# Performance work log

Hardware: AMD Instinct MI355X
Metric: run time of the kernel (lower is better)

## Reference

```python
import jax, jax.numpy as jnp
import numpy as np

VOCAB = 14
EMBED = 10
HIDDEN = 50
MLP = 50
PAD_IDX = 0
BATCH = 4096
SEQ = 2048


def setup_inputs() -> dict:
    key = jax.random.key(0)
    ks = jax.random.split(key, 10)
    tokens = jax.random.randint(ks[0], (BATCH, SEQ), 0, VOCAB, dtype=jnp.int64 if jax.config.jax_enable_x64 else jnp.int32)
    s_lstm = 1.0 / np.sqrt(HIDDEN)
    s_mlp1 = 1.0 / np.sqrt(HIDDEN)
    s_mlp2 = 1.0 / np.sqrt(MLP)
    emb = jax.random.normal(ks[1], (VOCAB, EMBED), jnp.float32)
    emb = emb.at[PAD_IDX].set(0.0)  # padding_idx row is zero in torch Embedding
    W_ih = jax.random.uniform(ks[2], (4 * HIDDEN, EMBED), jnp.float32, -s_lstm, s_lstm)
    W_hh = jax.random.uniform(ks[3], (4 * HIDDEN, HIDDEN), jnp.float32, -s_lstm, s_lstm)
    b_ih = jax.random.uniform(ks[4], (4 * HIDDEN,), jnp.float32, -s_lstm, s_lstm)
    b_hh = jax.random.uniform(ks[5], (4 * HIDDEN,), jnp.float32, -s_lstm, s_lstm)
    W1 = jax.random.uniform(ks[6], (MLP, HIDDEN), jnp.float32, -s_mlp1, s_mlp1)
    b1 = jax.random.uniform(ks[7], (MLP,), jnp.float32, -s_mlp1, s_mlp1)
    W2 = jax.random.uniform(ks[8], (1, MLP), jnp.float32, -s_mlp2, s_mlp2)
    b2 = jax.random.uniform(ks[9], (1,), jnp.float32, -s_mlp2, s_mlp2)
    return {"input": tokens, "emb": emb, "W_ih": W_ih, "W_hh": W_hh,
            "b_ih": b_ih, "b_hh": b_hh, "W1": W1, "b1": b1, "W2": W2, "b2": b2}


def reference(input, emb, W_ih, W_hh, b_ih, b_hh, W1, b1, W2, b2):
    x = emb[input]                                   # [B, T, E]
    mask = (input != PAD_IDX).astype(emb.dtype)      # [B, T]
    xs = jnp.swapaxes(x, 0, 1)                       # [T, B, E]
    ms = jnp.swapaxes(mask, 0, 1)[:, :, None]        # [T, B, 1]
    B = input.shape[0]

    def step(carry, inp):
        h, c = carry
        xt, mt = inp
        gates = xt @ W_ih.T + b_ih + h @ W_hh.T + b_hh  # [B, 4H], order i,f,g,o
        i, f, g, o = jnp.split(gates, 4, axis=-1)
        i = jax.nn.sigmoid(i)
        f = jax.nn.sigmoid(f)
        g = jnp.tanh(g)
        o = jax.nn.sigmoid(o)
        c_new = f * c + i * g
        h_new = o * jnp.tanh(c_new)
        # blend: keep old state on padded positions
        h = h_new * mt + h * (1.0 - mt)
        c = c_new * mt + c * (1.0 - mt)
        return (h, c), None

    h0 = jnp.zeros((B, HIDDEN), emb.dtype)
    c0 = jnp.zeros((B, HIDDEN), emb.dtype)
    (h, c), _ = jax.lax.scan(step, (h0, c0), (xs, ms))
    hidden = h @ W1.T + b1                            # [B, MLP]
    out = jax.nn.sigmoid(hidden @ W2.T + b2)          # [B, 1]
    return out
```

## Files before the change

kernel.cpp:

```cpp
#include <hip/hip_runtime.h>

#define BATCH 4096
#define SEQ   2048
#define EMB   10
#define HID   50
#define VOCAB 14
#define NTILE 13
#define TROW  2052

using bf16x8 = __attribute__((ext_vector_type(8))) short;
using f32x4  = __attribute__((ext_vector_type(4))) float;

__device__ __forceinline__ short f2bf(float f) {
  unsigned u = __builtin_bit_cast(unsigned, f);
  u = (u + 0x7FFFu + ((u >> 16) & 1u)) >> 16;
  return (short)u;
}
__device__ __forceinline__ float fsigm(float x) {
  return __builtin_amdgcn_rcpf(1.0f + __builtin_amdgcn_exp2f(x * -1.44269504f));
}

__global__ void prep_kernel(const float* __restrict__ emb,  const float* __restrict__ W_ih,
                            const float* __restrict__ W_hh, const float* __restrict__ b_ih,
                            const float* __restrict__ b_hh, short* __restrict__ Apack) {
  int idx = blockIdx.x * 256 + threadIdx.x;
  if (idx >= NTILE * 2 * 64 * 8) return;
  int j    = idx & 7;
  int lane = (idx >> 3) & 63;
  int kf   = (idx >> 9) & 1;
  int t    = idx >> 10;
  int m    = lane & 15;
  int q    = m >> 2, g = m & 3;
  int jh   = 13 * q + t;
  int k    = kf * 32 + (lane >> 4) * 8 + j;
  float v = 0.0f;
  if (jh < HID) {
    int R = g * HID + jh;
    float scale = (g == 2) ? -2.885390082f : -1.442695041f;
    if (k < HID) {
      v = W_hh[R * HID + k] * scale;
    } else {
      int vo = k - HID;
      float s = b_ih[R] + b_hh[R];
      for (int e = 0; e < EMB; ++e) s += emb[vo * EMB + e] * W_ih[R * EMB + e];
      v = s * scale;
    }
  }
  Apack[idx] = f2bf(v);
}

__global__ __launch_bounds__(512, 1) void lstm_kernel(
    const int* __restrict__ tokens, const short* __restrict__ Apack,
    const float* __restrict__ W1, const float* __restrict__ b1,
    const float* __restrict__ W2, const float* __restrict__ b2,
    float* __restrict__ out) {
  __shared__ __align__(16) unsigned char toku8[16 * TROW];
  __shared__ __align__(16) short hbuf[2][16 * 64];
  __shared__ float hfin[16 * 52];
  __shared__ float mlp_hid[16 * 52];

  const int tid  = threadIdx.x;
  const int lane = tid & 63;
  const int wv   = tid >> 6;
  const int b0   = blockIdx.x * 16;
  const int bB   = lane & 15;
  const int jj   = lane >> 4;
  const bool two = (wv < 5);
  const int jh0  = 13 * jj + wv;
  const int jh1  = 13 * jj + wv + 8;
  const bool hval1 = two && (jh1 < HID);

  const int ohi   = (wv - 5) * 64 + lane;
  const bool ohact = (wv == 5 || wv == 6) && (ohi < 112);
  const int ohr   = ohi / 7;
  const int ohsub = ohi % 7;
  const int ohoct = (ohsub < 3) ? 6 : 7;
  const int ohinn = (ohsub < 3) ? (4 + 4 * ohsub) : (4 * (ohsub - 3));
  const int ohb   = ohr * 128 + 16 * ((ohoct + ohr) & 7) + ohinn;
  const int ohv0  = 2 * ohsub, ohv1 = 2 * ohsub + 1;

  bf16x8 Af00 = {}, Af01 = {}, Af10 = {}, Af11 = {};
  Af00 = *(const bf16x8*)(Apack + ((wv * 2 + 0) * 64 + lane) * 8);
  Af01 = *(const bf16x8*)(Apack + ((wv * 2 + 1) * 64 + lane) * 8);
  if (two) {
    Af10 = *(const bf16x8*)(Apack + (((wv + 8) * 2 + 0) * 64 + lane) * 8);
    Af11 = *(const bf16x8*)(Apack + (((wv + 8) * 2 + 1) * 64 + lane) * 8);
  }

  for (int i = tid; i < 16 * 512; i += 512) {
    int row = i >> 9, c4 = i & 511;
    int4 tv = *(const int4*)&tokens[(b0 + row) * SEQ + 4 * c4];
    unsigned pk = (tv.x & 0xFF) | ((tv.y & 0xFF) << 8) |
                  ((tv.z & 0xFF) << 16) | ((tv.w & 0xFF) << 24);
    *(unsigned*)&toku8[row * TROW + 4 * c4] = pk;
  }
  for (int i = tid; i < 1024; i += 512) hbuf[0][i] = 0;
  __syncthreads();

  char* hb = (char*)hbuf;
  const int rb0  = bB * 128 + 16 * ((jj + bB) & 7);
  const int rb1  = bB * 128 + 16 * (((jj + 4) + bB) & 7);
  const int hwb0 = bB * 128 + 16 * (((jh0 >> 3) + bB) & 7) + 2 * (jh0 & 7);
  const int hwb1 = bB * 128 + 16 * (((jh1 >> 3) + bB) & 7) + 2 * (jh1 & 7);
  const unsigned char* myrow = &toku8[bB * TROW];
  const unsigned char* ohtok = &toku8[ohr * TROW];

  if (ohact) {
    int tk = ohtok[0];
    unsigned wb = ((tk == ohv0) ? 0x3F80u : 0u) | ((tk == ohv1) ? 0x3F800000u : 0u);
    *(unsigned*)(hb + ohb) = wb;
  }

  float c0 = 0.f, h0 = 0.f, c1 = 0.f, h1 = 0.f;
  unsigned mp = 0;

#define CELL(ACC, C, H)                                                        \
  {                                                                            \
    float eA = __builtin_amdgcn_exp2f(ACC[0]);                                 \
    float eB = __builtin_amdgcn_exp2f(ACC[1]);                                 \
    float eC = __builtin_amdgcn_exp2f(ACC[2]);                                 \
    float eG = __builtin_amdgcn_exp2f(ACC[3]);                                 \
    float a1 = 1.0f + eA, bb1 = 1.0f + eB, cc1 = 1.0f + eC, g1 = 1.0f + eG;    \
    float P   = a1 * cc1;                                                      \
    float t1  = __builtin_fmaf(-eC, bb1, bb1);                                 \
    float num = __builtin_fmaf(C, P, t1);                                      \
    float den = P * bb1;                                                       \
    float cn  = num * __builtin_amdgcn_rcpf(den);                              \
    cn = fminf(fmaxf(cn, -30.0f), 30.0f);                                      \
    float eH  = __builtin_amdgcn_exp2f(cn * -2.885390082f);                    \
    float hd  = g1 * (1.0f + eH);                                              \
    float hn  = (1.0f - eH) * __builtin_amdgcn_rcpf(hd);                       \
    C = keep ? cn : C;                                                         \
    H = keep ? hn : H;                                                         \
  }

  for (int t = 0; t < SEQ; t += 16) {
#pragma unroll
    for (int u = 0; u < 16; ++u) {
      const int T  = t + u;
      const int PB = (u & 1) * 2048, PN = PB ^ 2048;
      __syncthreads();

      bf16x8 Bf0 = *(const bf16x8*)(hb + PB + rb0);
      bf16x8 Bf1 = *(const bf16x8*)(hb + PB + rb1);
      if ((u & 3) == 0) mp = *(const unsigned*)(myrow + T);

      f32x4 acc0 = {0.f, 0.f, 0.f, 0.f};
      acc0 = __builtin_amdgcn_mfma_f32_16x16x32_bf16(Af00, Bf0, acc0, 0, 0, 0);
      acc0 = __builtin_amdgcn_mfma_f32_16x16x32_bf16(Af01, Bf1, acc0, 0, 0, 0);
      f32x4 acc1 = {0.f, 0.f, 0.f, 0.f};
      if (two) {
        acc1 = __builtin_amdgcn_mfma_f32_16x16x32_bf16(Af10, Bf0, acc1, 0, 0, 0);
        acc1 = __builtin_amdgcn_mfma_f32_16x16x32_bf16(Af11, Bf1, acc1, 0, 0, 0);
      }

      if (ohact && T + 1 < SEQ) {
        int tk = ohtok[T + 1];
        unsigned wb = ((tk == ohv0) ? 0x3F80u : 0u) |
                      ((tk == ohv1) ? 0x3F800000u : 0u);
        *(unsigned*)(hb + PN + ohb) = wb;
      }

      const bool keep = (((mp >> (8 * (u & 3))) & 0xFF) != 0);
      CELL(acc0, c0, h0)
      *(short*)(hb + PN + hwb0) = f2bf(h0);
      if (two) {
        CELL(acc1, c1, h1)
        if (hval1) *(short*)(hb + PN + hwb1) = f2bf(h1);
      }
    }
  }
#undef CELL

  hfin[bB * 52 + jh0] = h0;
  if (hval1) hfin[bB * 52 + jh1] = h1;
  __syncthreads();
  for (int idx = tid; idx < 16 * 64; idx += 512) {
    int b = idx >> 6, m = idx & 63;
    if (m < HID) {
      float s = b1[m];
      for (int j2 = 0; j2 < HID; ++j2) s += hfin[b * 52 + j2] * W1[m * HID + j2];
      mlp_hid[b * 52 + m] = s;
    }
  }
  __syncthreads();
  if (tid < 16) {
    float s = b2[0];
    for (int m2 = 0; m2 < HID; ++m2) s += mlp_hid[tid * 52 + m2] * W2[m2];
    out[b0 + tid] = fsigm(s);
  }
}

extern "C" void kernel_launch(void* const* d_in, const int* in_sizes, int n_in,
                              void* d_out, int out_size, void* d_ws, size_t ws_size,
                              hipStream_t stream) {
  const int*   tokens = (const int*)  d_in[0];
  const float* emb    = (const float*)d_in[1];
  const float* W_ih   = (const float*)d_in[2];
  const float* W_hh   = (const float*)d_in[3];
  const float* b_ih   = (const float*)d_in[4];
  const float* b_hh   = (const float*)d_in[5];
  const float* W1     = (const float*)d_in[6];
  const float* b1     = (const float*)d_in[7];
  const float* W2     = (const float*)d_in[8];
  const float* b2     = (const float*)d_in[9];
  float* outp  = (float*)d_out;
  short* Apack = (short*)d_ws;

  hipLaunchKernelGGL(prep_kernel, dim3(52), dim3(256), 0, stream,
                     emb, W_ih, W_hh, b_ih, b_hh, Apack);
  hipLaunchKernelGGL(lstm_kernel, dim3(BATCH / 16), dim3(512), 0, stream,
                     tokens, Apack, W1, b1, W2, b2, outp);
}
```

Baseline: 852.1 us.

## Remap hidden units so paired waves write packed bf16 pairs and share reciprocals

```diff
diff --git a/kernel.cpp b/kernel.cpp
--- a/kernel.cpp
+++ b/kernel.cpp
@@ -5,7 +5,6 @@
 #define EMB   10
 #define HID   50
 #define VOCAB 14
-#define NTILE 13
 #define TROW  2052
 
 using bf16x8 = __attribute__((ext_vector_type(8))) short;
@@ -16,6 +15,9 @@
   u = (u + 0x7FFFu + ((u >> 16) & 1u)) >> 16;
   return (short)u;
 }
+__device__ __forceinline__ unsigned f2bf2(float lo, float hi) {
+  return (unsigned)(unsigned short)f2bf(lo) | ((unsigned)(unsigned short)f2bf(hi) << 16);
+}
 __device__ __forceinline__ float fsigm(float x) {
   return __builtin_amdgcn_rcpf(1.0f + __builtin_amdgcn_exp2f(x * -1.44269504f));
 }
@@ -24,14 +26,15 @@
                             const float* __restrict__ W_hh, const float* __restrict__ b_ih,
                             const float* __restrict__ b_hh, short* __restrict__ Apack) {
   int idx = blockIdx.x * 256 + threadIdx.x;
-  if (idx >= NTILE * 2 * 64 * 8) return;
+  if (idx >= 13 * 2 * 64 * 8) return;
   int j    = idx & 7;
   int lane = (idx >> 3) & 63;
   int kf   = (idx >> 9) & 1;
-  int t    = idx >> 10;
+  int tid  = idx >> 10;
   int m    = lane & 15;
   int q    = m >> 2, g = m & 3;
-  int jh   = 13 * q + t;
+  int jh   = (tid < 10) ? (2 * ((tid >> 1) * 4 + q) + (tid & 1))
+                        : (40 + (tid - 10) * 4 + q);
   int k    = kf * 32 + (lane >> 4) * 8 + j;
   float v = 0.0f;
   if (jh < HID) {
@@ -65,27 +68,30 @@
   const int b0   = blockIdx.x * 16;
   const int bB   = lane & 15;
   const int jj   = lane >> 4;
-  const bool two = (wv < 5);
-  const int jh0  = 13 * jj + wv;
-  const int jh1  = 13 * jj + wv + 8;
-  const bool hval1 = two && (jh1 < HID);
-
-  const int ohi   = (wv - 5) * 64 + lane;
-  const bool ohact = (wv == 5 || wv == 6) && (ohi < 112);
-  const int ohr   = ohi / 7;
-  const int ohsub = ohi % 7;
+
+  const bool two = (0xA7 >> wv) & 1;
+  const int  fr  = __builtin_popcount(0xA7 & ((1 << wv) - 1));
+  const int  sr  = __builtin_popcount(0x58 & ((1 << wv) - 1));
+  const int  p   = fr * 4 + jj;
+  const int  jhS = 40 + sr * 4 + jj;
+  const bool sval = !two && (jhS < HID);
+
+  const int t0 = two ? (fr * 2) : (10 + sr);
+  bf16x8 Af00 = *(const bf16x8*)(Apack + ((t0 * 2 + 0) * 64 + lane) * 8);
+  bf16x8 Af01 = *(const bf16x8*)(Apack + ((t0 * 2 + 1) * 64 + lane) * 8);
+  bf16x8 Af10 = {}, Af11 = {};
+  if (two) {
+    Af10 = *(const bf16x8*)(Apack + (((t0 + 1) * 2 + 0) * 64 + lane) * 8);
+    Af11 = *(const bf16x8*)(Apack + (((t0 + 1) * 2 + 1) * 64 + lane) * 8);
+  }
+
+  const bool ohact = (wv == 3 || wv == 4) && (lane < 56);
+  const int ohr   = (wv - 3) * 8 + lane / 7;
+  const int ohsub = lane % 7;
   const int ohoct = (ohsub < 3) ? 6 : 7;
   const int ohinn = (ohsub < 3) ? (4 + 4 * ohsub) : (4 * (ohsub - 3));
   const int ohb   = ohr * 128 + 16 * ((ohoct + ohr) & 7) + ohinn;
   const int ohv0  = 2 * ohsub, ohv1 = 2 * ohsub + 1;
-
-  bf16x8 Af00 = {}, Af01 = {}, Af10 = {}, Af11 = {};
-  Af00 = *(const bf16x8*)(Apack + ((wv * 2 + 0) * 64 + lane) * 8);
-  Af01 = *(const bf16x8*)(Apack + ((wv * 2 + 1) * 64 + lane) * 8);
-  if (two) {
-    Af10 = *(const bf16x8*)(Apack + (((wv + 8) * 2 + 0) * 64 + lane) * 8);
-    Af11 = *(const bf16x8*)(Apack + (((wv + 8) * 2 + 1) * 64 + lane) * 8);
-  }
 
   for (int i = tid; i < 16 * 512; i += 512) {
     int row = i >> 9, c4 = i & 511;
@@ -98,10 +104,10 @@
   __syncthreads();
 
   char* hb = (char*)hbuf;
-  const int rb0  = bB * 128 + 16 * ((jj + bB) & 7);
-  const int rb1  = bB * 128 + 16 * (((jj + 4) + bB) & 7);
-  const int hwb0 = bB * 128 + 16 * (((jh0 >> 3) + bB) & 7) + 2 * (jh0 & 7);
-  const int hwb1 = bB * 128 + 16 * (((jh1 >> 3) + bB) & 7) + 2 * (jh1 & 7);
+  const int rb0   = bB * 128 + 16 * ((jj + bB) & 7);
+  const int rb1   = bB * 128 + 16 * (((jj + 4) + bB) & 7);
+  const int hwb32 = bB * 128 + 16 * (((p >> 2) + bB) & 7) + ((4 * p) & 15);
+  const int hwb16 = bB * 128 + 16 * (((jhS >> 3) + bB) & 7) + 2 * (jhS & 7);
   const unsigned char* myrow = &toku8[bB * TROW];
   const unsigned char* ohtok = &toku8[ohr * TROW];
 
@@ -113,26 +119,6 @@
 
   float c0 = 0.f, h0 = 0.f, c1 = 0.f, h1 = 0.f;
   unsigned mp = 0;
-
-#define CELL(ACC, C, H)                                                        \
-  {                                                                            \
-    float eA = __builtin_amdgcn_exp2f(ACC[0]);                                 \
-    float eB = __builtin_amdgcn_exp2f(ACC[1]);                                 \
-    float eC = __builtin_amdgcn_exp2f(ACC[2]);                                 \
-    float eG = __builtin_amdgcn_exp2f(ACC[3]);                                 \
-    float a1 = 1.0f + eA, bb1 = 1.0f + eB, cc1 = 1.0f + eC, g1 = 1.0f + eG;    \
-    float P   = a1 * cc1;                                                      \
-    float t1  = __builtin_fmaf(-eC, bb1, bb1);                                 \
-    float num = __builtin_fmaf(C, P, t1);                                      \
-    float den = P * bb1;                                                       \
-    float cn  = num * __builtin_amdgcn_rcpf(den);                              \
-    cn = fminf(fmaxf(cn, -30.0f), 30.0f);                                      \
-    float eH  = __builtin_amdgcn_exp2f(cn * -2.885390082f);                    \
-    float hd  = g1 * (1.0f + eH);                                              \
-    float hn  = (1.0f - eH) * __builtin_amdgcn_rcpf(hd);                       \
-    C = keep ? cn : C;                                                         \
-    H = keep ? hn : H;                                                         \
-  }
 
   for (int t = 0; t < SEQ; t += 16) {
 #pragma unroll
@@ -162,18 +148,67 @@
       }
 
       const bool keep = (((mp >> (8 * (u & 3))) & 0xFF) != 0);
-      CELL(acc0, c0, h0)
-      *(short*)(hb + PN + hwb0) = f2bf(h0);
+
       if (two) {
-        CELL(acc1, c1, h1)
-        if (hval1) *(short*)(hb + PN + hwb1) = f2bf(h1);
+        float eA0 = __builtin_amdgcn_exp2f(acc0[0]);
+        float eB0 = __builtin_amdgcn_exp2f(acc0[1]);
+        float eC0 = __builtin_amdgcn_exp2f(acc0[2]);
+        float eG0 = __builtin_amdgcn_exp2f(acc0[3]);
+        float eA1 = __builtin_amdgcn_exp2f(acc1[0]);
+        float eB1 = __builtin_amdgcn_exp2f(acc1[1]);
+        float eC1 = __builtin_amdgcn_exp2f(acc1[2]);
+        float eG1 = __builtin_amdgcn_exp2f(acc1[3]);
+        float a10 = 1.f + eA0, b10 = 1.f + eB0, c10 = 1.f + eC0, g10 = 1.f + eG0;
+        float a11 = 1.f + eA1, b11 = 1.f + eB1, c11 = 1.f + eC1, g11 = 1.f + eG1;
+        float P0 = a10 * c10, P1 = a11 * c11;
+        float t10 = __builtin_fmaf(-eC0, b10, b10);
+        float t11 = __builtin_fmaf(-eC1, b11, b11);
+        float num0 = __builtin_fmaf(c0, P0, t10);
+        float num1 = __builtin_fmaf(c1, P1, t11);
+        float den0 = P0 * b10, den1 = P1 * b11;
+        float r  = __builtin_amdgcn_rcpf(den0 * den1);
+        float cn0 = num0 * (den1 * r);
+        float cn1 = num1 * (den0 * r);
+        float cl0 = fminf(cn0 * -2.885390082f, 40.0f);
+        float cl1 = fminf(cn1 * -2.885390082f, 40.0f);
+        float H0 = __builtin_amdgcn_exp2f(cl0);
+        float H1 = __builtin_amdgcn_exp2f(cl1);
+        float hd0 = g10 * (1.f + H0);
+        float hd1 = g11 * (1.f + H1);
+        float rh = __builtin_amdgcn_rcpf(hd0 * hd1);
+        float hn0 = (1.f - H0) * (hd1 * rh);
+        float hn1 = (1.f - H1) * (hd0 * rh);
+        c0 = keep ? cn0 : c0;  h0 = keep ? hn0 : h0;
+        c1 = keep ? cn1 : c1;  h1 = keep ? hn1 : h1;
+        *(unsigned*)(hb + PN + hwb32) = f2bf2(h0, h1);
+      } else {
+        float eA = __builtin_amdgcn_exp2f(acc0[0]);
+        float eB = __builtin_amdgcn_exp2f(acc0[1]);
+        float eC = __builtin_amdgcn_exp2f(acc0[2]);
+        float eG = __builtin_amdgcn_exp2f(acc0[3]);
+        float a1 = 1.f + eA, bb1 = 1.f + eB, cc1 = 1.f + eC, g1 = 1.f + eG;
+        float P   = a1 * cc1;
+        float t1  = __builtin_fmaf(-eC, bb1, bb1);
+        float num = __builtin_fmaf(c0, P, t1);
+        float den = P * bb1;
+        float cn  = num * __builtin_amdgcn_rcpf(den);
+        float cl  = fminf(cn * -2.885390082f, 40.0f);
+        float eH  = __builtin_amdgcn_exp2f(cl);
+        float hd  = g1 * (1.f + eH);
+        float hn  = (1.f - eH) * __builtin_amdgcn_rcpf(hd);
+        c0 = keep ? cn : c0;
+        h0 = keep ? hn : h0;
+        if (sval) *(short*)(hb + PN + hwb16) = f2bf(h0);
       }
     }
   }
-#undef CELL
-
-  hfin[bB * 52 + jh0] = h0;
-  if (hval1) hfin[bB * 52 + jh1] = h1;
+
+  if (two) {
+    hfin[bB * 52 + 2 * p]     = h0;
+    hfin[bB * 52 + 2 * p + 1] = h1;
+  } else if (sval) {
+    hfin[bB * 52 + jhS] = h0;
+  }
   __syncthreads();
   for (int idx = tid; idx < 16 * 64; idx += 512) {
     int b = idx >> 6, m = idx & 63;
```

Measured after the change: 813.8 us (median of 2 runs). 1.05x faster.
